# Performance work log

Hardware: AMD Instinct MI355X
Metric: run time of the kernel (lower is better)

## Reference

```python
import jax, jax.numpy as jnp
import numpy as np

N_NODES = 100_000
N_EDGES = 3_200_000
HIDDEN = 16


def setup_inputs() -> dict:
    key = jax.random.key(0)
    k1, k2, k3, k4 = jax.random.split(key, 4)
    x = jax.random.normal(k1, (N_NODES, 3), dtype=jnp.float32)
    edge_index = jax.random.randint(k2, (2, N_EDGES), 0, N_NODES, dtype=jnp.int32)
    # Glorot-style init for the two GCN layers (PyG GCNConv: lin weight + bias)
    W1 = jax.random.normal(k3, (3, HIDDEN), dtype=jnp.float32) * (1.0 / np.sqrt(3.0))
    b1 = jnp.zeros((HIDDEN,), dtype=jnp.float32)
    W2 = jax.random.normal(k4, (HIDDEN, 1), dtype=jnp.float32) * (1.0 / np.sqrt(HIDDEN))
    b2 = jnp.zeros((1,), dtype=jnp.float32)
    return {"x": x, "edge_index": edge_index, "W1": W1, "b1": b1, "W2": W2, "b2": b2}


def reference(x, edge_index, W1, b1, W2, b2):
    n = x.shape[0]  # static under jit
    # GCNConv default: add self-loops, symmetric degree normalization
    self_loop = jnp.arange(n, dtype=edge_index.dtype)
    src = jnp.concatenate([edge_index[0], self_loop])
    dst = jnp.concatenate([edge_index[1], self_loop])
    deg = jax.ops.segment_sum(jnp.ones_like(src, dtype=x.dtype), dst, num_segments=n)
    inv_sqrt_deg = jnp.where(deg > 0, jax.lax.rsqrt(jnp.maximum(deg, 1.0)), 0.0)
    norm = inv_sqrt_deg[src] * inv_sqrt_deg[dst]  # [E+N]

    def gcn_conv(h, W, b):
        h = h @ W  # linear transform first (cheaper: small out dim)
        msg = norm[:, None] * h[src]  # gather + scale
        return jax.ops.segment_sum(msg, dst, num_segments=n) + b  # scatter-add

    h = jax.nn.relu(gcn_conv(x, W1, b1))
    out = gcn_conv(h, W2, b2)
    return out.squeeze(-1)  # [N]
```

## Files before the change

### kernel.cpp

```cpp
#include <hip/hip_runtime.h>

#define HIDDEN 16
#define CB 1024
#define CB_SHIFT 10
#define NCB_MAX 512
#define CHUNK 4096
#define BT 1024
#define SPL 8


__global__ void k_hist(const int* __restrict__ dst, int e, int ncb, int nchunk,
                       unsigned int* __restrict__ hcT) {
    __shared__ unsigned int h[NCB_MAX];
    for (int i = threadIdx.x; i < ncb; i += blockDim.x) h[i] = 0u;
    __syncthreads();
    int start = blockIdx.x * CHUNK;
    int end = min(start + CHUNK, e);
    int i = start + threadIdx.x;
    for (; i + 3 * 256 < end; i += 4 * 256) {
        unsigned d0 = dst[i], d1 = dst[i + 256], d2 = dst[i + 512], d3 = dst[i + 768];
        atomicAdd(&h[d0 >> CB_SHIFT], 1u);
        atomicAdd(&h[d1 >> CB_SHIFT], 1u);
        atomicAdd(&h[d2 >> CB_SHIFT], 1u);
        atomicAdd(&h[d3 >> CB_SHIFT], 1u);
    }
    for (; i < end; i += 256)
        atomicAdd(&h[((unsigned)dst[i]) >> CB_SHIFT], 1u);
    __syncthreads();
    for (int j = threadIdx.x; j < ncb; j += blockDim.x)
        hcT[(size_t)j * nchunk + blockIdx.x] = h[j];
}

__global__ void k_scanf(unsigned int* __restrict__ hcT,
                        unsigned int* __restrict__ cntc, int nchunk) {
    __shared__ unsigned int ts[256];
    __shared__ unsigned int carry;
    int b = blockIdx.x, t = threadIdx.x;
    if (t == 0) carry = 0u;
    __syncthreads();
    size_t row = (size_t)b * nchunk;
    for (int t0 = 0; t0 < nchunk; t0 += 256) {
        int i = t0 + t;
        unsigned int v = (i < nchunk) ? hcT[row + i] : 0u;
        ts[t] = v;
        __syncthreads();
        for (int off = 1; off < 256; off <<= 1) {
            unsigned int u = (t >= off) ? ts[t - off] : 0u;
            __syncthreads();
            ts[t] += u;
            __syncthreads();
        }
        if (i < nchunk) hcT[row + i] = carry + ts[t] - v;
        __syncthreads();
        if (t == 0) carry += ts[255];
        __syncthreads();
    }
    if (t == 0) cntc[b] = carry;
}

__global__ __launch_bounds__(256) void
k_scanb(const unsigned int* __restrict__ cntc, int ncb,
        unsigned int* __restrict__ basec,
        unsigned int* __restrict__ rowptr, int n, unsigned int e) {
    __shared__ unsigned int tsum[256];
    int t = threadIdx.x;
    unsigned int s = (t < ncb) ? cntc[t] : 0u;
    tsum[t] = s;
    __syncthreads();
    for (int off = 1; off < 256; off <<= 1) {
        unsigned int v = (t >= off) ? tsum[t - off] : 0u;
        __syncthreads();
        tsum[t] += v;
        __syncthreads();
    }
    if (t < ncb) basec[t] = tsum[t] - s;
    if (t == 255) basec[ncb] = tsum[255];
    if (t == 0) rowptr[n] = e;
}

__global__ void k_fill(const int* __restrict__ src, const int* __restrict__ dst,
                       int e, int ncb, int nchunk,
                       const unsigned int* __restrict__ basec,
                       const unsigned int* __restrict__ hcT,
                       unsigned int* __restrict__ tmp) {
    __shared__ unsigned int h[NCB_MAX];
    __shared__ unsigned int lb[NCB_MAX];
    for (int j = threadIdx.x; j < ncb; j += blockDim.x) {
        lb[j] = basec[j] + hcT[(size_t)j * nchunk + blockIdx.x];
        h[j] = 0u;
    }
    __syncthreads();
    int start = blockIdx.x * CHUNK;
    int end = min(start + CHUNK, e);
    for (int i = start + threadIdx.x; i < end; i += 256) {
        unsigned int d = (unsigned)dst[i];
        unsigned int s = (unsigned)src[i];
        unsigned int b = d >> CB_SHIFT;
        unsigned int r = atomicAdd(&h[b], 1u);
        tmp[lb[b] + r] = (s << CB_SHIFT) | (d & (CB - 1u));
    }
}

__global__ __launch_bounds__(BT) void
k_sortC(const unsigned int* __restrict__ tmp,
        const unsigned int* __restrict__ basec,
        const float* __restrict__ x,
        unsigned int* __restrict__ rowptr, unsigned int* __restrict__ tmp2,
        float4* __restrict__ xs4, int n) {
    __shared__ unsigned int cnt[CB];
    __shared__ unsigned int sc[CB];
    __shared__ unsigned int cur[CB];
    int t = threadIdx.x, b = blockIdx.x;
    unsigned int s = basec[b], endp = basec[b + 1];
    cnt[t] = 0u;
    __syncthreads();
    for (unsigned int i = s + t; i < endp; i += BT)
        atomicAdd(&cnt[tmp[i] & (CB - 1u)], 1u);
    __syncthreads();
    sc[t] = cnt[t];
    __syncthreads();
    for (int off = 1; off < CB; off <<= 1) {
        unsigned int v = (t >= off) ? sc[t - off] : 0u;
        __syncthreads();
        sc[t] += v;
        __syncthreads();
    }
    unsigned int excl = sc[t] - cnt[t];
    cur[t] = s + excl;
    int node = (b << CB_SHIFT) + t;
    if (node < n) {
        rowptr[node] = s + excl;
        float iv = rsqrtf((float)(1u + cnt[t]));
        xs4[node] = make_float4(x[3 * node] * iv, x[3 * node + 1] * iv,
                                x[3 * node + 2] * iv, iv);
    }
    __syncthreads();
    for (unsigned int i = s + t; i < endp; i += BT) {
        unsigned int rec = tmp[i];
        unsigned int r = atomicAdd(&cur[rec & (CB - 1u)], 1u);
        tmp2[r] = rec >> CB_SHIFT;
    }
}

__global__ void k_s1(const unsigned int* __restrict__ rowptr,
                     const unsigned int* __restrict__ tmp2,
                     const float4* __restrict__ xs4,
                     const float* __restrict__ W1, const float* __restrict__ b1,
                     const float* __restrict__ W2, const float* __restrict__ b2,
                     float* __restrict__ t2s, float* __restrict__ out, int n) {
    int gid = blockIdx.x * blockDim.x + threadIdx.x;
    int i = gid >> 1, h = gid & 1;
    bool valid = (i < n);
    unsigned int s = 0, epos = 0;
    if (valid) { s = rowptr[i]; epos = rowptr[i + 1]; }
    unsigned int half = (epos - s) >> 1;
    unsigned int b0 = h ? s + half : s;
    unsigned int b1r = h ? epos : s + half;
    float v0 = 0.f, v1 = 0.f, v2 = 0.f;
    unsigned int j = b0;
    for (; j + 4 <= b1r; j += 4) {
        unsigned a0 = tmp2[j], a1 = tmp2[j + 1], a2 = tmp2[j + 2], a3 = tmp2[j + 3];
        float4 p0 = xs4[a0], p1 = xs4[a1], p2 = xs4[a2], p3 = xs4[a3];
        v0 += (p0.x + p1.x) + (p2.x + p3.x);
        v1 += (p0.y + p1.y) + (p2.y + p3.y);
        v2 += (p0.z + p1.z) + (p2.z + p3.z);
    }
    for (; j < b1r; j++) {
        float4 p = xs4[tmp2[j]];
        v0 += p.x; v1 += p.y; v2 += p.z;
    }
    v0 += __shfl_xor(v0, 1);
    v1 += __shfl_xor(v1, 1);
    v2 += __shfl_xor(v2, 1);
    if (valid && h == 0) {
        float4 me = xs4[i];
        float iv = me.w;
        v0 = (v0 + me.x) * iv;
        v1 = (v1 + me.y) * iv;
        v2 = (v2 + me.z) * iv;
        float acc = 0.f;
#pragma unroll
        for (int k = 0; k < HIDDEN; k++) {
            float hh = fmaxf(fmaf(v0, W1[k], fmaf(v1, W1[HIDDEN + k],
                            fmaf(v2, W1[2 * HIDDEN + k], b1[k]))), 0.f);
            acc += hh * W2[k];
        }
        t2s[i] = acc * iv;
        out[i] = b2[0] + acc * iv * iv;
    }
}

__global__ void k_s2(const unsigned int* __restrict__ rowptr,
                     const unsigned int* __restrict__ tmp2,
                     const float* __restrict__ t2s, const float4* __restrict__ xs4,
                     float* __restrict__ out, int n) {
    int gid = blockIdx.x * blockDim.x + threadIdx.x;
    int i = gid >> 1, h = gid & 1;
    bool valid = (i < n);
    unsigned int s = 0, epos = 0;
    if (valid) { s = rowptr[i]; epos = rowptr[i + 1]; }
    unsigned int half = (epos - s) >> 1;
    unsigned int b0 = h ? s + half : s;
    unsigned int b1r = h ? epos : s + half;
    float v = 0.f;
    unsigned int j = b0;
    for (; j + 4 <= b1r; j += 4) {
        unsigned a0 = tmp2[j], a1 = tmp2[j + 1], a2 = tmp2[j + 2], a3 = tmp2[j + 3];
        v += (t2s[a0] + t2s[a1]) + (t2s[a2] + t2s[a3]);
    }
    for (; j < b1r; j++) v += t2s[tmp2[j]];
    v += __shfl_xor(v, 1);
    if (valid && h == 0) out[i] += v * xs4[i].w;
}


__global__ void k_zero(unsigned int* a, int na) {
    int i = blockIdx.x * blockDim.x + threadIdx.x;
    if (i < na) a[i] = 0u;
}
__global__ __launch_bounds__(BT) void
k_deg_split(const unsigned int* __restrict__ tmp, const unsigned int* __restrict__ basec,
            const unsigned int* __restrict__ cntc, unsigned int* __restrict__ deg, int n) {
    __shared__ unsigned int degl[CB];
    int t = threadIdx.x;
    degl[t] = 0u;
    __syncthreads();
    int b = blockIdx.x / SPL, sl = blockIdx.x % SPL;
    unsigned int s = basec[b], m = cntc[b];
    for (unsigned int i = sl * BT + t; i < m; i += SPL * BT)
        atomicAdd(&degl[tmp[s + i] & (CB - 1u)], 1u);
    __syncthreads();
    int node = b * CB + t;
    unsigned int c = degl[t];
    if (node < n && c) atomicAdd(&deg[node], c);
}
__global__ void k_inv_s(const unsigned int* __restrict__ deg, const float* __restrict__ x,
                        float4* __restrict__ xs4, int n) {
    int i = blockIdx.x * blockDim.x + threadIdx.x;
    if (i >= n) return;
    float iv = rsqrtf((float)(deg[i] + 1u));
    xs4[i] = make_float4(x[3 * i] * iv, x[3 * i + 1] * iv, x[3 * i + 2] * iv, iv);
}
__global__ __launch_bounds__(BT) void
k_s1_split(const unsigned int* __restrict__ tmp, const unsigned int* __restrict__ basec,
           const unsigned int* __restrict__ cntc, const float4* __restrict__ xs4,
           float* __restrict__ agg0, float* __restrict__ agg1, float* __restrict__ agg2, int n) {
    __shared__ float a0[CB], a1[CB], a2[CB];
    int t = threadIdx.x;
    a0[t] = 0.f; a1[t] = 0.f; a2[t] = 0.f;
    __syncthreads();
    int b = blockIdx.x / SPL, sl = blockIdx.x % SPL;
    unsigned int s = basec[b], m = cntc[b];
    for (unsigned int i = sl * BT + t; i < m; i += SPL * BT) {
        unsigned rec = tmp[s + i];
        float4 v = xs4[rec >> CB_SHIFT];
        unsigned dl = rec & (CB - 1u);
        atomicAdd(&a0[dl], v.x); atomicAdd(&a1[dl], v.y); atomicAdd(&a2[dl], v.z);
    }
    __syncthreads();
    int node = b * CB + t;
    if (node < n) {
        if (a0[t] != 0.f) atomicAdd(&agg0[node], a0[t]);
        if (a1[t] != 0.f) atomicAdd(&agg1[node], a1[t]);
        if (a2[t] != 0.f) atomicAdd(&agg2[node], a2[t]);
    }
}
__global__ void k_epi_s(const float* __restrict__ agg0, const float* __restrict__ agg1,
                        const float* __restrict__ agg2, const float4* __restrict__ xs4,
                        const float* __restrict__ W1, const float* __restrict__ b1,
                        const float* __restrict__ W2, const float* __restrict__ b2,
                        float* __restrict__ t2s, float* __restrict__ out, int n) {
    int i = blockIdx.x * blockDim.x + threadIdx.x;
    if (i >= n) return;
    float4 xv = xs4[i];
    float iv = xv.w;
    float v0 = iv * (agg0[i] + xv.x), v1 = iv * (agg1[i] + xv.y), v2 = iv * (agg2[i] + xv.z);
    float acc = 0.f;
#pragma unroll
    for (int j = 0; j < HIDDEN; j++) {
        float h = fmaxf(fmaf(v0, W1[j], fmaf(v1, W1[HIDDEN + j],
                       fmaf(v2, W1[2 * HIDDEN + j], b1[j]))), 0.f);
        acc += h * W2[j];
    }
    t2s[i] = acc * iv;
    out[i] = b2[0] + acc * iv * iv;
}
__global__ __launch_bounds__(BT) void
k_s2_split(const unsigned int* __restrict__ tmp, const unsigned int* __restrict__ basec,
           const unsigned int* __restrict__ cntc, const float* __restrict__ t2s,
           const float4* __restrict__ xs4, float* __restrict__ out, int n) {
    __shared__ float o[CB];
    int t = threadIdx.x;
    o[t] = 0.f;
    __syncthreads();
    int b = blockIdx.x / SPL, sl = blockIdx.x % SPL;
    unsigned int s = basec[b], m = cntc[b];
    for (unsigned int i = sl * BT + t; i < m; i += SPL * BT) {
        unsigned rec = tmp[s + i];
        atomicAdd(&o[rec & (CB - 1u)], t2s[rec >> CB_SHIFT]);
    }
    __syncthreads();
    int node = b * CB + t;
    if (node < n && o[t] != 0.f) atomicAdd(&out[node], o[t] * xs4[node].w);
}


extern "C" void kernel_launch(void* const* d_in, const int* in_sizes, int n_in,
                              void* d_out, int out_size, void* d_ws, size_t ws_size,
                              hipStream_t stream) {
    const float* x  = (const float*)d_in[0];
    const int*   ei = (const int*)d_in[1];
    const float* W1 = (const float*)d_in[2];
    const float* b1 = (const float*)d_in[3];
    const float* W2 = (const float*)d_in[4];
    const float* b2 = (const float*)d_in[5];
    float* out = (float*)d_out;

    int n = in_sizes[0] / 3;
    int e = in_sizes[1] / 2;
    const int* src = ei;
    const int* dst = ei + e;
    const int B = 256;

    int ncb = (n + CB - 1) / CB;
    int nchunk = (e + CHUNK - 1) / CHUNK;
    int gridN2 = (2 * n + B - 1) / B;

    size_t needc = (size_t)n * 16 + (size_t)n * 4 + (size_t)(n + 1) * 4
                 + (size_t)(2 * ncb + 1) * 4 + (size_t)ncb * nchunk * 4
                 + (size_t)e * 8 + 64;

    if (ncb <= 256 && n < (1 << 21) && ws_size >= needc) {
        float4* xs4 = (float4*)d_ws;
        float* t2s = (float*)(xs4 + n);
        unsigned int* rowptr = (unsigned int*)(t2s + n);
        unsigned int* cntc   = rowptr + (n + 1);
        unsigned int* basec  = cntc + ncb;
        unsigned int* hcT    = basec + ncb + 1;
        unsigned int* tmp    = hcT + (size_t)ncb * nchunk;
        unsigned int* tmp2   = tmp + e;

        k_hist<<<nchunk, B, 0, stream>>>(dst, e, ncb, nchunk, hcT);
        k_scanf<<<ncb, B, 0, stream>>>(hcT, cntc, nchunk);
        k_scanb<<<1, B, 0, stream>>>(cntc, ncb, basec, rowptr, n, (unsigned)e);
        k_fill<<<nchunk, B, 0, stream>>>(src, dst, e, ncb, nchunk, basec, hcT, tmp);
        k_sortC<<<ncb, BT, 0, stream>>>(tmp, basec, x, rowptr, tmp2, xs4, n);
        k_s1<<<gridN2, B, 0, stream>>>(rowptr, tmp2, xs4, W1, b1, W2, b2, t2s, out, n);
        k_s2<<<gridN2, B, 0, stream>>>(rowptr, tmp2, t2s, xs4, out, n);
    } else {
        int gridN = (n + B - 1) / B;
        float4* xs4 = (float4*)d_ws;
        float* agg0 = (float*)(xs4 + n);
        float* agg1 = agg0 + n;
        float* agg2 = agg1 + n;
        unsigned int* deg = (unsigned int*)(agg2 + n);
        float* t2s = (float*)(deg + n);
        unsigned int* cntc   = (unsigned int*)(t2s + n);
        unsigned int* basec  = cntc + ncb;
        unsigned int* hcT    = basec + ncb + 1;
        unsigned int* tmp    = hcT + (size_t)ncb * nchunk;

        k_zero<<<(4 * n + B - 1) / B, B, 0, stream>>>((unsigned int*)agg0, 4 * n);
        k_hist<<<nchunk, B, 0, stream>>>(dst, e, ncb, nchunk, hcT);
        k_scanf<<<ncb, B, 0, stream>>>(hcT, cntc, nchunk);
        k_scanb<<<1, B, 0, stream>>>(cntc, ncb, basec, (unsigned int*)t2s, 0, (unsigned)e);
        k_fill<<<nchunk, B, 0, stream>>>(src, dst, e, ncb, nchunk, basec, hcT, tmp);
        k_deg_split<<<ncb * SPL, BT, 0, stream>>>(tmp, basec, cntc, deg, n);
        k_inv_s<<<gridN, B, 0, stream>>>(deg, x, xs4, n);
        k_s1_split<<<ncb * SPL, BT, 0, stream>>>(tmp, basec, cntc, xs4, agg0, agg1, agg2, n);
        k_epi_s<<<gridN, B, 0, stream>>>(agg0, agg1, agg2, xs4, W1, b1, W2, b2, t2s, out, n);
        k_s2_split<<<ncb * SPL, BT, 0, stream>>>(tmp, basec, cntc, t2s, xs4, out, n);
    }
}
```

Before: 193.0 us.

## Split per-bucket counting sort into count kernel and sub-partitioned scatter kernel

The fused per-coarse-bucket sort kernel is split into a counting/prefix kernel that writes rowptr and scaled features, and a separate scatter kernel launched with SUBP blocks per bucket, each handling one slice of destination nodes. ncb is only about 98 buckets for 100k nodes, so this is meant to raise the block count above the GPU's CU count and improve occupancy. In exchange each bucket's records are read SUBP more times, and there is an extra kernel launch.

```diff
diff --git a/kernel.cpp b/kernel.cpp
--- a/kernel.cpp
+++ b/kernel.cpp
@@ -6,6 +6,8 @@
 #define NCB_MAX 512
 #define CHUNK 4096
 #define BT 1024
+#define SUBP 8
+#define SUBW (CB / SUBP)
 #define SPL 8
 
 
@@ -102,14 +104,12 @@
 }
 
 __global__ __launch_bounds__(BT) void
-k_sortC(const unsigned int* __restrict__ tmp,
-        const unsigned int* __restrict__ basec,
-        const float* __restrict__ x,
-        unsigned int* __restrict__ rowptr, unsigned int* __restrict__ tmp2,
-        float4* __restrict__ xs4, int n) {
+k_cnt(const unsigned int* __restrict__ tmp,
+      const unsigned int* __restrict__ basec,
+      const float* __restrict__ x,
+      unsigned int* __restrict__ rowptr, float4* __restrict__ xs4, int n) {
     __shared__ unsigned int cnt[CB];
     __shared__ unsigned int sc[CB];
-    __shared__ unsigned int cur[CB];
     int t = threadIdx.x, b = blockIdx.x;
     unsigned int s = basec[b], endp = basec[b + 1];
     cnt[t] = 0u;
@@ -125,20 +125,37 @@
         sc[t] += v;
         __syncthreads();
     }
-    unsigned int excl = sc[t] - cnt[t];
-    cur[t] = s + excl;
     int node = (b << CB_SHIFT) + t;
     if (node < n) {
-        rowptr[node] = s + excl;
+        rowptr[node] = s + sc[t] - cnt[t];
         float iv = rsqrtf((float)(1u + cnt[t]));
         xs4[node] = make_float4(x[3 * node] * iv, x[3 * node + 1] * iv,
                                 x[3 * node + 2] * iv, iv);
     }
-    __syncthreads();
+}
+
+__global__ __launch_bounds__(BT) void
+k_scat(const unsigned int* __restrict__ tmp,
+       const unsigned int* __restrict__ basec,
+       const unsigned int* __restrict__ rowptr,
+       unsigned int* __restrict__ tmp2, int n) {
+    __shared__ unsigned int cur[SUBW];
+    int t = threadIdx.x;
+    int b = blockIdx.x / SUBP, p = blockIdx.x % SUBP;
+    unsigned int lo = p * SUBW;
+    if (t < SUBW) {
+        int node = (b << CB_SHIFT) + lo + t;
+        cur[t] = (node < n) ? rowptr[node] : 0u;
+    }
+    __syncthreads();
+    unsigned int s = basec[b], endp = basec[b + 1];
     for (unsigned int i = s + t; i < endp; i += BT) {
         unsigned int rec = tmp[i];
-        unsigned int r = atomicAdd(&cur[rec & (CB - 1u)], 1u);
-        tmp2[r] = rec >> CB_SHIFT;
+        unsigned int dl = rec & (CB - 1u);
+        if (dl - lo < SUBW) {
+            unsigned int r = atomicAdd(&cur[dl - lo], 1u);
+            tmp2[r] = rec >> CB_SHIFT;
+        }
     }
 }
 
@@ -344,7 +361,8 @@
         k_scanf<<<ncb, B, 0, stream>>>(hcT, cntc, nchunk);
         k_scanb<<<1, B, 0, stream>>>(cntc, ncb, basec, rowptr, n, (unsigned)e);
         k_fill<<<nchunk, B, 0, stream>>>(src, dst, e, ncb, nchunk, basec, hcT, tmp);
-        k_sortC<<<ncb, BT, 0, stream>>>(tmp, basec, x, rowptr, tmp2, xs4, n);
+        k_cnt<<<ncb, BT, 0, stream>>>(tmp, basec, x, rowptr, xs4, n);
+        k_scat<<<ncb * SUBP, BT, 0, stream>>>(tmp, basec, rowptr, tmp2, n);
         k_s1<<<gridN2, B, 0, stream>>>(rowptr, tmp2, xs4, W1, b1, W2, b2, t2s, out, n);
         k_s2<<<gridN2, B, 0, stream>>>(rowptr, tmp2, t2s, xs4, out, n);
     } else {
```

Result: no change. 196.7 us (+1.9%).
